# Kernel tuning notes

Hardware: AMD Instinct MI355X
Metric: run time of the kernel (lower is better)

The kernel has to match this reference:

```python
import jax, jax.numpy as jnp
import numpy as np

BATCH = 8
MAX_SEQ = 2048
HEAD_NUM = 16  # num_attention_heads_per_partition


def setup_inputs() -> dict:
    key = jax.random.key(0)
    k1, k2 = jax.random.split(key)
    attention_mask = jax.random.uniform(k1, (BATCH, 1, MAX_SEQ, MAX_SEQ), dtype=jnp.float16)
    # ragged per-sequence lengths in [1, MAX_SEQ]; concrete (shape params, not traced)
    seq_lengths = np.asarray(jax.random.randint(k2, (BATCH,), 1, MAX_SEQ + 1), dtype=np.int32)
    return {"attention_mask": attention_mask, "seq_lengths": seq_lengths}


def reference(attention_mask, seq_lengths):
    # Pack the top-left s_i x s_i block of each batch's mask, replicated across
    # HEAD_NUM heads, into one flat fp16 buffer; then threshold > 0.5 -> bool.
    mask = attention_mask.astype(jnp.float16)
    lens = [int(s) for s in np.asarray(seq_lengths)]  # static shape params
    pieces = []
    for i, s in enumerate(lens):
        block = mask[i, 0, :s, :s]                        # [s, s]
        rep = jnp.broadcast_to(block, (HEAD_NUM, s, s))   # replicate per head
        pieces.append(rep.reshape(-1))                    # [HEAD_NUM*s*s]
    packed = jnp.concatenate(pieces)                      # [sum_i HEAD_NUM*s_i^2]
    return packed > jnp.float16(0.5)
```

## Files before the change

kernel.cpp:

```cpp
#include <hip/hip_runtime.h>

typedef int i4  __attribute__((ext_vector_type(4)));
typedef int i2  __attribute__((ext_vector_type(2)));
typedef int i4u __attribute__((ext_vector_type(4), aligned(4)));

#define THREADS 256
#define WAVES_PB 4
#define K1_BLOCKS 4096
#define K1_ITERS 2
#define K2_BLOCKS 8192
#define PK_OFF 256
#define WS_NEED ((size_t)4 * (PK_OFF + 32768u * 1024u))

__global__ void setup_offsets_kernel(const int* __restrict__ seq,
                                     unsigned int* __restrict__ ws) {
    if (threadIdx.x == 0 && blockIdx.x == 0) {
        unsigned int o16 = 0, cs = 0;
        ws[0] = 0u; ws[9] = 0u;
        for (int b = 0; b < 8; ++b) {
            unsigned int s  = (unsigned int)seq[b];
            unsigned int s2 = s * s;
            o16 += 16u * s2;
            cs  += (s2 + 1023u) >> 10;
            ws[1 + b]  = o16;
            ws[10 + b] = cs;
            ws[18 + b] = s;
            ws[26 + b] = s2;
            ((float*)ws)[34 + b] = 1.0f / (float)s;
        }
    }
}


__global__ void __launch_bounds__(THREADS)
pack_kernel(const float* __restrict__ mask, const unsigned int* __restrict__ ws,
            int* __restrict__ pk) {
    __shared__ unsigned int csum[9];
    __shared__ unsigned int slen[8];
    __shared__ unsigned int ssq[8];
    __shared__ float        sinv[8];
    int tx = threadIdx.x;
    if (tx < 9) csum[tx] = ws[9 + tx];
    if (tx < 8) {
        slen[tx] = ws[18 + tx];
        ssq[tx]  = ws[26 + tx];
        sinv[tx] = ((const float*)ws)[34 + tx];
    }
    __syncthreads();

    unsigned int nchunks     = csum[8];
    unsigned int total_waves = gridDim.x * WAVES_PB;
    unsigned int wave_id     = blockIdx.x * WAVES_PB + ((unsigned int)tx >> 6);
    unsigned int lane        = (unsigned int)tx & 63u;

#pragma unroll 1
    for (int it = 0; it < K1_ITERS; ++it) {
        unsigned int chunk = wave_id + (unsigned int)it * total_waves;
        if (chunk >= nchunks) break;

        unsigned int b = 0;
#pragma unroll
        for (int j = 1; j < 8; ++j) b += (chunk >= csum[j]) ? 1u : 0u;

        unsigned int s   = slen[b];
        unsigned int s2  = ssq[b];
        float        inv = sinv[b];
        unsigned int p0  = (chunk - csum[b]) << 10;
        unsigned int pb  = csum[b] << 10;
        const float* mb  = mask + ((size_t)b << 22);

#pragma unroll
        for (int sub = 0; sub < 4; ++sub) {
            unsigned int p = p0 + ((unsigned int)sub << 8) + (lane << 2);
            if (p + 4u <= s2) {
                unsigned int row = (unsigned int)((float)p * inv);
                int col = (int)p - (int)(row * s);
                if (col < 0)            { row -= 1u; col += (int)s; }
                else if (col >= (int)s) { row += 1u; col -= (int)s; }
                unsigned int r0 = row;  int c0 = col;
                float v0 = mb[(size_t)r0 * 2048u + (unsigned int)c0];
                c0++; if (c0 == (int)s) { c0 = 0; r0++; }
                float v1 = mb[(size_t)r0 * 2048u + (unsigned int)c0];
                c0++; if (c0 == (int)s) { c0 = 0; r0++; }
                float v2 = mb[(size_t)r0 * 2048u + (unsigned int)c0];
                c0++; if (c0 == (int)s) { c0 = 0; r0++; }
                float v3 = mb[(size_t)r0 * 2048u + (unsigned int)c0];
                i4 o = (i4){(v0 > 0.5f) ? 1 : 0, (v1 > 0.5f) ? 1 : 0,
                            (v2 > 0.5f) ? 1 : 0, (v3 > 0.5f) ? 1 : 0};
                *(i4*)(pk + pb + p) = o;
            } else {
#pragma unroll
                for (int j = 0; j < 4; ++j) {
                    unsigned int pp = p + (unsigned int)j;
                    if (pp >= s2) continue;
                    unsigned int row = (unsigned int)((float)pp * inv);
                    int col = (int)pp - (int)(row * s);
                    if (col < 0)            { row -= 1u; col += (int)s; }
                    else if (col >= (int)s) { row += 1u; col -= (int)s; }
                    float v = mb[(size_t)row * 2048u + (unsigned int)col];
                    pk[pb + pp] = (v > 0.5f) ? 1 : 0;
                }
            }
        }
    }
}

__global__ void __launch_bounds__(THREADS)
fanout_kernel(const unsigned int* __restrict__ ws, const int* __restrict__ pk,
              int* __restrict__ out) {
    __shared__ unsigned int off16[9];
    __shared__ unsigned int csum[9];
    __shared__ unsigned int ssq[8];
    int tx = threadIdx.x;
    if (tx < 9) { off16[tx] = ws[tx]; csum[tx] = ws[9 + tx]; }
    if (tx < 8) ssq[tx] = ws[26 + tx];
    __syncthreads();

    unsigned int nitems      = csum[8] << 4;
    unsigned int total_waves = gridDim.x * WAVES_PB;
    unsigned int W           = blockIdx.x * WAVES_PB + ((unsigned int)tx >> 6);
    unsigned int lane        = (unsigned int)tx & 63u;

#pragma unroll 1
    for (unsigned int item = W; item < nitems; item += total_waves) {
        unsigned int cid = item >> 4;
        unsigned int h   = item & 15u;

        unsigned int b = 0;
#pragma unroll
        for (int j = 1; j < 8; ++j) b += (cid >= csum[j]) ? 1u : 0u;

        unsigned int s2 = ssq[b];
        unsigned int c  = cid - csum[b];
        const int*  srcb = pk + (csum[b] << 10);

        unsigned int hb   = off16[b] + h * s2;
        unsigned int lo   = hb + (c << 10);
        unsigned int clen = s2 - (c << 10);
        if (clen > 1024u) clen = 1024u;
        unsigned int hi = lo + clen;

        unsigned int qs = (lo + 3u) >> 2;
        unsigned int qe = hi >> 2;

#pragma unroll
        for (int k = 0; k < 4; ++k) {
            unsigned int q = qs + lane + ((unsigned int)k << 6);
            if (q < qe) {
                i4 v = *(const i4u*)(srcb + ((q << 2) - hb));
                *(i4*)(out + ((size_t)q << 2)) = v;
            }
        }
        if (lane < 3u) {
            unsigned int e = lo + lane;
            if (e < hi && e < (qs << 2)) out[e] = srcb[e - hb];
            unsigned int e2 = (qe << 2) + lane;
            if (e2 >= lo && e2 < hi) out[e2] = srcb[e2 - hb];
        }
    }
}


#define STORE_SHIFT(VV, SIG) do {                                              \
    *(i4*)(out + offh + 0   + (SIG)) = VV[0];                                  \
    *(i4*)(out + offh + 256 + (SIG)) = VV[1];                                  \
    *(i4*)(out + offh + 512 + (SIG)) = VV[2];                                  \
    if (lane < 63u) *(i4*)(out + offh + 768 + (SIG)) = VV[3];                  \
    if (lane == 0u) {                                                          \
        out[habase] = o[0].x;                                                  \
        if ((SIG) >= 2) out[habase + 1] = o[0].y;                              \
        if ((SIG) == 3) out[habase + 2] = o[0].z;                              \
    }                                                                          \
    if (lane == 63u) {                                                         \
        if ((SIG) == 1) out[habase + 1021] = o[3].y;                           \
        if ((SIG) <= 2) out[habase + 1022] = o[3].z;                           \
        out[habase + 1023] = o[3].w;                                           \
    }                                                                          \
} while (0)

__global__ void __launch_bounds__(THREADS)
unpad_mask_kernel_fb(const float* __restrict__ mask,
                     const unsigned int* __restrict__ ws,
                     int* __restrict__ out) {
    __shared__ unsigned int off16[9];
    __shared__ unsigned int csum[9];
    __shared__ unsigned int slen[8];
    __shared__ unsigned int ssq[8];
    __shared__ float        sinv[8];

    int tx = threadIdx.x;
    if (tx < 9) { off16[tx] = ws[tx]; csum[tx] = ws[9 + tx]; }
    if (tx < 8) {
        slen[tx] = ws[18 + tx];
        ssq[tx]  = ws[26 + tx];
        sinv[tx] = ((const float*)ws)[34 + tx];
    }
    __syncthreads();

    unsigned int nchunks     = csum[8];
    unsigned int total_waves = gridDim.x * WAVES_PB;
    unsigned int wave_id     = blockIdx.x * WAVES_PB + ((unsigned int)tx >> 6);
    unsigned int lane        = (unsigned int)tx & 63u;

#pragma unroll 1
    for (int it = 0; it < K1_ITERS; ++it) {
        unsigned int chunk = wave_id + (unsigned int)it * total_waves;
        if (chunk >= nchunks) break;

        unsigned int b = 0;
#pragma unroll
        for (int j = 1; j < 8; ++j) b += (chunk >= csum[j]) ? 1u : 0u;

        unsigned int s    = slen[b];
        unsigned int s2   = ssq[b];
        float        inv  = sinv[b];
        unsigned int p0   = (chunk - csum[b]) << 10;
        unsigned int base = off16[b];
        const float* mb   = mask + ((size_t)b << 22);

        if (s2 - p0 >= 1024u) {
            unsigned int q0 = p0 + (lane << 2);
            i4 o[4];
#pragma unroll
            for (int sub = 0; sub < 4; ++sub) {
                unsigned int q   = q0 + ((unsigned int)sub << 8);
                unsigned int row = (unsigned int)((float)q * inv);
                int col = (int)q - (int)(row * s);
                if (col < 0)            { row -= 1u; col += (int)s; }
                else if (col >= (int)s) { row += 1u; col -= (int)s; }
                unsigned int r0 = row;  int c0 = col;
                float v0 = mb[(size_t)r0 * 2048u + (unsigned int)c0];
                c0++; if (c0 == (int)s) { c0 = 0; r0++; }
                float v1 = mb[(size_t)r0 * 2048u + (unsigned int)c0];
                c0++; if (c0 == (int)s) { c0 = 0; r0++; }
                float v2 = mb[(size_t)r0 * 2048u + (unsigned int)c0];
                c0++; if (c0 == (int)s) { c0 = 0; r0++; }
                float v3 = mb[(size_t)r0 * 2048u + (unsigned int)c0];
                o[sub] = (i4){(v0 > 0.5f) ? 1 : 0, (v1 > 0.5f) ? 1 : 0,
                              (v2 > 0.5f) ? 1 : 0, (v3 > 0.5f) ? 1 : 0};
            }

            if ((s & 1u) == 0u) {
                unsigned int off = base + q0;
#pragma unroll
                for (int h = 0; h < 16; ++h) {
                    *(i4*)(out + off)       = o[0];
                    *(i4*)(out + off + 256) = o[1];
                    *(i4*)(out + off + 512) = o[2];
                    *(i4*)(out + off + 768) = o[3];
                    off += s2;
                }
            } else {
                int src = ((int)lane + 1) & 63;
                int sel = (lane == 0u) ? 1 : 0;
                int e0x = sel ? o[1].x : o[0].x;
                int e0y = sel ? o[1].y : o[0].y;
                int e0z = sel ? o[1].z : o[0].z;
                int e1x = sel ? o[2].x : o[1].x;
                int e1y = sel ? o[2].y : o[1].y;
                int e1z = sel ? o[2].z : o[1].z;
                int e2x = sel ? o[3].x : o[2].x;
                int e2y = sel ? o[3].y : o[2].y;
                int e2z = sel ? o[3].z : o[2].z;
                int n0x = __shfl(e0x, src, 64), n0y = __shfl(e0y, src, 64), n0z = __shfl(e0z, src, 64);
                int n1x = __shfl(e1x, src, 64), n1y = __shfl(e1y, src, 64), n1z = __shfl(e1z, src, 64);
                int n2x = __shfl(e2x, src, 64), n2y = __shfl(e2y, src, 64), n2z = __shfl(e2z, src, 64);
                int n3x = __shfl(o[3].x, src, 64), n3y = __shfl(o[3].y, src, 64), n3z = __shfl(o[3].z, src, 64);

                i4 v1[4], v2[4], v3[4];
                v1[0] = (i4){o[0].y, o[0].z, o[0].w, n0x};
                v1[1] = (i4){o[1].y, o[1].z, o[1].w, n1x};
                v1[2] = (i4){o[2].y, o[2].z, o[2].w, n2x};
                v1[3] = (i4){o[3].y, o[3].z, o[3].w, n3x};
                v2[0] = (i4){o[0].z, o[0].w, n0x, n0y};
                v2[1] = (i4){o[1].z, o[1].w, n1x, n1y};
                v2[2] = (i4){o[2].z, o[2].w, n2x, n2y};
                v2[3] = (i4){o[3].z, o[3].w, n3x, n3y};
                v3[0] = (i4){o[0].w, n0x, n0y, n0z};
                v3[1] = (i4){o[1].w, n1x, n1y, n1z};
                v3[2] = (i4){o[2].w, n2x, n2y, n2z};
                v3[3] = (i4){o[3].w, n3x, n3y, n3z};

                unsigned int habase = base + p0;
#pragma unroll
                for (int h = 0; h < 16; ++h) {
                    unsigned int offh = habase + (lane << 2);
                    const int r0c = h & 3;
                    if (r0c == 0) {
                        *(i4*)(out + offh)       = o[0];
                        *(i4*)(out + offh + 256) = o[1];
                        *(i4*)(out + offh + 512) = o[2];
                        *(i4*)(out + offh + 768) = o[3];
                    } else if (r0c == 1) {
                        STORE_SHIFT(v3, 3);
                    } else if (r0c == 2) {
                        STORE_SHIFT(v2, 2);
                    } else {
                        STORE_SHIFT(v1, 1);
                    }
                    habase += s2;
                }
            }
        } else {
#pragma unroll 1
            for (int sub = 0; sub < 4; ++sub) {
                unsigned int sp0 = p0 + ((unsigned int)sub << 8);
                if (sp0 >= s2) break;
#pragma unroll
                for (int j = 0; j < 4; ++j) {
                    unsigned int p = sp0 + (lane << 2) + (unsigned int)j;
                    if (p >= s2) continue;
                    unsigned int row = (unsigned int)((float)p * inv);
                    int col = (int)p - (int)(row * s);
                    if (col < 0)            { row -= 1u; col += (int)s; }
                    else if (col >= (int)s) { row += 1u; col -= (int)s; }
                    float v = mb[(size_t)row * 2048u + (unsigned int)col];
                    int o = (v > 0.5f) ? 1 : 0;
                    unsigned int off = base + p;
#pragma unroll
                    for (int h = 0; h < 16; ++h) {
                        out[off] = o;
                        off += s2;
                    }
                }
            }
        }
    }
}

extern "C" void kernel_launch(void* const* d_in, const int* in_sizes, int n_in,
                              void* d_out, int out_size, void* d_ws, size_t ws_size,
                              hipStream_t stream) {
    const float*  mask = (const float*)d_in[0];
    const int*    seq  = (const int*)d_in[1];
    unsigned int* ws   = (unsigned int*)d_ws;
    int*          out  = (int*)d_out;

    setup_offsets_kernel<<<1, 64, 0, stream>>>(seq, ws);
    if (ws_size >= WS_NEED) {
        int* pk = (int*)ws + PK_OFF;
        pack_kernel<<<K1_BLOCKS, THREADS, 0, stream>>>(mask, ws, pk);
        fanout_kernel<<<K2_BLOCKS, THREADS, 0, stream>>>(ws, pk, out);
    } else {
        unpad_mask_kernel_fb<<<K1_BLOCKS, THREADS, 0, stream>>>(mask, ws, out);
    }
}
```

Before: 724.6 us.

## Replace chunk-per-head fanout with contiguous output-range sweep per block

The fanout kernel, which copied each packed 1024-element chunk once per head, is replaced by a sweep kernel. In the new kernel each of 512 blocks owns a contiguous, 16K-aligned range of the output and walks it in 1024-element windows, finding batch and head by division. Full windows use four unrolled 16-byte copies per lane, and windows that cross a head or batch boundary use a loop with scalar edge handling. The goal is sequential, coalesced output writes with fewer blocks. The cost is per-window divisions and possible load imbalance at the last block.

```diff
diff --git a/kernel.cpp b/kernel.cpp
--- a/kernel.cpp
+++ b/kernel.cpp
@@ -1,28 +1,27 @@
 #include <hip/hip_runtime.h>
 
 typedef int i4  __attribute__((ext_vector_type(4)));
-typedef int i2  __attribute__((ext_vector_type(2)));
 typedef int i4u __attribute__((ext_vector_type(4), aligned(4)));
 
 #define THREADS 256
 #define WAVES_PB 4
 #define K1_BLOCKS 4096
 #define K1_ITERS 2
-#define K2_BLOCKS 8192
+#define SWEEP_BLOCKS 512
 #define PK_OFF 256
 #define WS_NEED ((size_t)4 * (PK_OFF + 32768u * 1024u))
 
 __global__ void setup_offsets_kernel(const int* __restrict__ seq,
                                      unsigned int* __restrict__ ws) {
     if (threadIdx.x == 0 && blockIdx.x == 0) {
-        unsigned int o16 = 0, cs = 0;
+        unsigned int oE = 0, cs = 0;
         ws[0] = 0u; ws[9] = 0u;
         for (int b = 0; b < 8; ++b) {
             unsigned int s  = (unsigned int)seq[b];
             unsigned int s2 = s * s;
-            o16 += 16u * s2;
-            cs  += (s2 + 1023u) >> 10;
-            ws[1 + b]  = o16;
+            oE += s2 << 4;
+            cs += (s2 + 1023u) >> 10;
+            ws[1 + b]  = oE;
             ws[10 + b] = cs;
             ws[18 + b] = s;
             ws[26 + b] = s2;
@@ -30,7 +29,6 @@
         }
     }
 }
-
 
 __global__ void __launch_bounds__(THREADS)
 pack_kernel(const float* __restrict__ mask, const unsigned int* __restrict__ ws,
@@ -106,56 +104,74 @@
 }
 
 __global__ void __launch_bounds__(THREADS)
-fanout_kernel(const unsigned int* __restrict__ ws, const int* __restrict__ pk,
-              int* __restrict__ out) {
-    __shared__ unsigned int off16[9];
+sweep_kernel(const unsigned int* __restrict__ ws, const int* __restrict__ pk,
+             int* __restrict__ out) {
+    __shared__ unsigned int offE[9];
     __shared__ unsigned int csum[9];
     __shared__ unsigned int ssq[8];
     int tx = threadIdx.x;
-    if (tx < 9) { off16[tx] = ws[tx]; csum[tx] = ws[9 + tx]; }
+    if (tx < 9) { offE[tx] = ws[tx]; csum[tx] = ws[9 + tx]; }
     if (tx < 8) ssq[tx] = ws[26 + tx];
     __syncthreads();
 
-    unsigned int nitems      = csum[8] << 4;
-    unsigned int total_waves = gridDim.x * WAVES_PB;
-    unsigned int W           = blockIdx.x * WAVES_PB + ((unsigned int)tx >> 6);
-    unsigned int lane        = (unsigned int)tx & 63u;
-
-#pragma unroll 1
-    for (unsigned int item = W; item < nitems; item += total_waves) {
-        unsigned int cid = item >> 4;
-        unsigned int h   = item & 15u;
-
-        unsigned int b = 0;
-#pragma unroll
-        for (int j = 1; j < 8; ++j) b += (cid >= csum[j]) ? 1u : 0u;
-
-        unsigned int s2 = ssq[b];
-        unsigned int c  = cid - csum[b];
-        const int*  srcb = pk + (csum[b] << 10);
-
-        unsigned int hb   = off16[b] + h * s2;
-        unsigned int lo   = hb + (c << 10);
-        unsigned int clen = s2 - (c << 10);
-        if (clen > 1024u) clen = 1024u;
-        unsigned int hi = lo + clen;
-
-        unsigned int qs = (lo + 3u) >> 2;
-        unsigned int qe = hi >> 2;
-
-#pragma unroll
-        for (int k = 0; k < 4; ++k) {
-            unsigned int q = qs + lane + ((unsigned int)k << 6);
-            if (q < qe) {
-                i4 v = *(const i4u*)(srcb + ((q << 2) - hb));
-                *(i4*)(out + ((size_t)q << 2)) = v;
-            }
-        }
-        if (lane < 3u) {
-            unsigned int e = lo + lane;
-            if (e < hi && e < (qs << 2)) out[e] = srcb[e - hb];
-            unsigned int e2 = (qe << 2) + lane;
-            if (e2 >= lo && e2 < hi) out[e2] = srcb[e2 - hb];
+    unsigned int Ntot = offE[8];
+    unsigned int R = ((Ntot + (unsigned int)SWEEP_BLOCKS - 1u) / (unsigned int)SWEEP_BLOCKS
+                      + 16383u) & ~16383u;
+    unsigned int blk_base = blockIdx.x * R;
+    if (blk_base >= Ntot) return;
+    unsigned int blk_end = blk_base + R;
+    if (blk_end > Ntot) blk_end = Ntot;
+
+    unsigned int wid  = (unsigned int)tx >> 6;
+    unsigned int lane = (unsigned int)tx & 63u;
+
+#pragma unroll 1
+    for (unsigned int c = wid; ; c += WAVES_PB) {
+        unsigned int x  = blk_base + (c << 10);
+        if (x >= blk_end) break;
+        unsigned int xe = x + 1024u;
+        if (xe > blk_end) xe = blk_end;
+
+#pragma unroll 1
+        while (x < xe) {
+            unsigned int b = 0;
+#pragma unroll
+            for (int j = 1; j < 8; ++j) b += (x >= offE[j]) ? 1u : 0u;
+            unsigned int s2    = ssq[b];
+            unsigned int local = x - offE[b];
+            unsigned int h     = local / s2;
+            unsigned int hb    = offE[b] + h * s2;
+            unsigned int send  = hb + s2;
+            if (send > xe) send = xe;
+            if (send <= x) break;
+            int delta = (int)(csum[b] << 10) - (int)hb;
+
+            if (send == x + 1024u) {
+                unsigned int q0 = (x >> 2) + lane;
+                i4 a0 = *(const i4u*)(pk + (int)(q0 << 2) + delta);
+                i4 a1 = *(const i4u*)(pk + (int)((q0 + 64u) << 2) + delta);
+                i4 a2 = *(const i4u*)(pk + (int)((q0 + 128u) << 2) + delta);
+                i4 a3 = *(const i4u*)(pk + (int)((q0 + 192u) << 2) + delta);
+                *(i4*)(out + ((q0) << 2))        = a0;
+                *(i4*)(out + ((q0 + 64u) << 2))  = a1;
+                *(i4*)(out + ((q0 + 128u) << 2)) = a2;
+                *(i4*)(out + ((q0 + 192u) << 2)) = a3;
+            } else {
+                unsigned int qs = (x + 3u) >> 2;
+                unsigned int qe = send >> 2;
+#pragma unroll 1
+                for (unsigned int q = qs + lane; q < qe; q += 64u) {
+                    i4 v = *(const i4u*)(pk + (int)(q << 2) + delta);
+                    *(i4*)(out + (q << 2)) = v;
+                }
+                if (lane < 3u) {
+                    unsigned int e = x + lane;
+                    if (e < send && e < (qs << 2)) out[e] = pk[(int)e + delta];
+                    unsigned int e2 = (qe << 2) + lane;
+                    if (e2 >= x && e2 < send) out[e2] = pk[(int)e2 + delta];
+                }
+            }
+            x = send;
         }
     }
 }
@@ -340,7 +356,7 @@
     if (ws_size >= WS_NEED) {
         int* pk = (int*)ws + PK_OFF;
         pack_kernel<<<K1_BLOCKS, THREADS, 0, stream>>>(mask, ws, pk);
-        fanout_kernel<<<K2_BLOCKS, THREADS, 0, stream>>>(ws, pk, out);
+        sweep_kernel<<<SWEEP_BLOCKS, THREADS, 0, stream>>>(ws, pk, out);
     } else {
         unpad_mask_kernel_fb<<<K1_BLOCKS, THREADS, 0, stream>>>(mask, ws, out);
     }
```

After: 732.3 us. About the same (+1.1%).
